# Performance work log

Hardware: AMD Instinct MI355X
Metric: run time of the kernel (lower is better)

The kernel has to match this reference:

```python
import jax, jax.numpy as jnp
import numpy as np

# dims: batch N, queries Q, frames F, patches-per-frame L, heads H, head_dim D
N, Q, F, L, H, D = 32, 64, 16, 196, 12, 64
E = H * D          # embed_dim = 768
K = F * L          # kv length = 3136


def setup_inputs() -> dict:
    key = jax.random.key(0)
    kq, kk, kv, km, kw1, kw2 = jax.random.split(key, 6)
    q = jax.random.normal(kq, (N, Q, E), dtype=jnp.float32)
    k = jax.random.normal(kk, (N, K, H, D), dtype=jnp.float32)
    v = jax.random.normal(kv, (N, K, H, D), dtype=jnp.float32)
    # frame-padding mask; guarantee >=1 valid patch per frame so the
    # per-frame softmax never sees an all -inf group (NaN otherwise)
    m = jax.random.bernoulli(km, 0.9, (N, K))
    m = m.reshape(N, F, L).at[:, :, 0].set(True).reshape(N, K)
    W_in = jax.random.normal(kw1, (E, E), dtype=jnp.float32) * 0.02   # in_proj (n_act=1)
    W_out = jax.random.normal(kw2, (E, E), dtype=jnp.float32) * 0.02  # out_proj
    return {"q": q, "k": k, "v": v, "m": m, "W_in": W_in, "W_out": W_out}


def reference(q, k, v, m, W_in, W_out):
    n, nq, e = q.shape
    h, d = H, e // H
    # in_proj (no bias) then split into heads; n_act == 1 so qs has one element
    qs = (q @ W_in.T).reshape(n, nq, h, d)
    # scaled QK affinity: [n, Q, K, h]
    aff = jnp.einsum('nqhc,nkhc->nqkh', qs * (d ** -0.5), k)
    # frame mask broadcast over queries and heads
    aff = jnp.where(m[:, None, :, None], aff, -jnp.inf)
    kn = aff.shape[2]
    # grouped softmax over patches within each frame (dim=-2 of the view)
    aff = jax.nn.softmax(aff.reshape(n, nq, F, kn // F, h), axis=-2)
    aff = aff.reshape(n, nq, kn, h)
    # mix with v and output projection
    mix = jnp.einsum('nqlh,nlhc->nqhc', aff, v)
    out = mix.reshape(n, nq, e) @ W_out.T
    # second return: stacked flattened qs, shape [n, n_act=1, Q, E]
    qs_out = qs.reshape(n, nq, e)[:, None]
    return out, qs_out
```

## Files before the change

### kernel.cpp

```cpp
#include <hip/hip_runtime.h>
#include <hip/hip_bf16.h>
#include <cfloat>

#define N_B 32
#define QN 64
#define FN 16
#define LP 196
#define HN 12
#define DH 64
#define EE 768
#define KLEN 3136
#define FPB 2
#define KROWS 208
#define VST 256

typedef short s16x4 __attribute__((ext_vector_type(4)));
typedef __bf16 bf16x8 __attribute__((ext_vector_type(8)));
typedef float f32x4 __attribute__((ext_vector_type(4)));
typedef unsigned u32x4 __attribute__((ext_vector_type(4)));

__device__ __forceinline__ bf16x8 cvt8(f32x4 a, f32x4 b) {
    bf16x8 r;
    r[0] = (__bf16)a[0]; r[1] = (__bf16)a[1]; r[2] = (__bf16)a[2]; r[3] = (__bf16)a[3];
    r[4] = (__bf16)b[0]; r[5] = (__bf16)b[1]; r[6] = (__bf16)b[2]; r[7] = (__bf16)b[3];
    return r;
}
__device__ __forceinline__ unsigned short bfb(float x) {
    return __builtin_bit_cast(unsigned short, (__bf16)x);
}
__device__ __forceinline__ unsigned pkbf(float lo, float hi) {
    return (unsigned)bfb(lo) | ((unsigned)bfb(hi) << 16);
}

__global__ __launch_bounds__(256) void gemm_mfma(const float* __restrict__ A,
                                                 const float* __restrict__ W,
                                                 float* __restrict__ C) {
    __shared__ unsigned short As[64 * 72];
    __shared__ unsigned short Ws[48 * 72];
    const int t = threadIdx.x;
    const int w = t >> 6, lane = t & 63, lr = lane & 15, lg = lane >> 4;
    const int m0 = blockIdx.x * 64;
    const int n0 = blockIdx.y * 48;

    f32x4 acc[3];
#pragma unroll
    for (int ct = 0; ct < 3; ++ct) acc[ct] = (f32x4){0.f, 0.f, 0.f, 0.f};

    for (int k0 = 0; k0 < EE; k0 += 32) {
        {
            int row = t >> 2, cb = t & 3;
            const float* src = A + (size_t)(m0 + row) * EE + k0 + cb * 8;
            f32x4 a = *(const f32x4*)src, b = *(const f32x4*)(src + 4);
            *(bf16x8*)&As[row * 72 + cb * 8] = cvt8(a, b);
        }
        if (t < 192) {
            int row = t >> 2, cb = t & 3;
            const float* src = W + (size_t)(n0 + row) * EE + k0 + cb * 8;
            f32x4 a = *(const f32x4*)src, b = *(const f32x4*)(src + 4);
            *(bf16x8*)&Ws[row * 72 + cb * 8] = cvt8(a, b);
        }
        __syncthreads();
        bf16x8 a = *(const bf16x8*)&As[(w * 16 + lr) * 72 + lg * 8];
#pragma unroll
        for (int ct = 0; ct < 3; ++ct) {
            bf16x8 b = *(const bf16x8*)&Ws[(ct * 16 + lr) * 72 + lg * 8];
            acc[ct] = __builtin_amdgcn_mfma_f32_16x16x32_bf16(a, b, acc[ct], 0, 0, 0);
        }
        __syncthreads();
    }
#pragma unroll
    for (int ct = 0; ct < 3; ++ct)
#pragma unroll
        for (int r = 0; r < 4; ++r)
            C[(size_t)(m0 + w * 16 + lg * 4 + r) * EE + n0 + ct * 16 + lr] = acc[ct][r];
}

__global__ __launch_bounds__(256) void zero_f32(float* __restrict__ p, int n4) {
    int i = blockIdx.x * 256 + threadIdx.x;
    if (i < n4) ((float4*)p)[i] = make_float4(0.f, 0.f, 0.f, 0.f);
}

__global__ __launch_bounds__(256, 2) void attn_mfma(const float* __restrict__ qs_g,
                                                    const float* __restrict__ k_g,
                                                    const float* __restrict__ v_g,
                                                    const int* __restrict__ m_g,
                                                    float* __restrict__ mix_g) {
    const int h = blockIdx.x, fg = blockIdx.y, n = blockIdx.z;

    __shared__ __attribute__((aligned(16))) unsigned short KV_s[64 * VST];
    __shared__ __attribute__((aligned(16))) float bias_s[224];

    const int t = threadIdx.x;
    const int w = t >> 6, lane = t & 63, lr = lane & 15, lg = lane >> 4;

    bf16x8 qb0, qb1;
    {
        const float* qp = qs_g + ((size_t)n * QN + w * 16 + lr) * EE + h * DH + lg * 8;
        f32x4 a = *(const f32x4*)qp, b = *(const f32x4*)(qp + 4);
        f32x4 c = *(const f32x4*)(qp + 32), d = *(const f32x4*)(qp + 36);
#pragma unroll
        for (int i = 0; i < 4; ++i) { a[i] *= 0.125f; b[i] *= 0.125f; c[i] *= 0.125f; d[i] *= 0.125f; }
        qb0 = cvt8(a, b);
        qb1 = cvt8(c, d);
    }

    float mix[4][4];
#pragma unroll
    for (int dt = 0; dt < 4; ++dt)
#pragma unroll
        for (int r = 0; r < 4; ++r) mix[dt][r] = 0.f;

    for (int ff = 0; ff < FPB; ++ff) {
        const size_t kbase = (size_t)n * KLEN + (size_t)(fg * FPB + ff) * LP;

        __syncthreads();

#pragma unroll
        for (int u = 0; u < 7; ++u) {
            int unit = t + 256 * u;
            if (unit < KROWS * 8) {
                int p = unit >> 3, blk = unit & 7;
                f32x4 a = {0.f, 0.f, 0.f, 0.f}, b = {0.f, 0.f, 0.f, 0.f};
                if (p < LP) {
                    const float* src = k_g + ((kbase + p) * HN + h) * DH + blk * 8;
                    a = *(const f32x4*)src;
                    b = *(const f32x4*)(src + 4);
                }
                *(bf16x8*)&KV_s[p * 64 + ((blk ^ (p & 7)) << 3)] = cvt8(a, b);
            }
        }
        if (t < 224) {
            float bv = -1e30f;
            if (t < LP && m_g[kbase + t] != 0) bv = 0.f;
            bias_s[t] = bv;
        }
        __syncthreads();

        f32x4 sc[13];
#pragma unroll
        for (int tl = 0; tl < 13; ++tl) {
            int row = tl * 16 + lr;
            bf16x8 a0 = *(const bf16x8*)&KV_s[row * 64 + ((lg ^ (lr & 7)) << 3)];
            bf16x8 a1 = *(const bf16x8*)&KV_s[row * 64 + (((4 + lg) ^ (lr & 7)) << 3)];
            f32x4 z = {0.f, 0.f, 0.f, 0.f};
            z = __builtin_amdgcn_mfma_f32_16x16x32_bf16(a0, qb0, z, 0, 0, 0);
            sc[tl] = __builtin_amdgcn_mfma_f32_16x16x32_bf16(a1, qb1, z, 0, 0, 0);
        }

        float mx = -FLT_MAX;
#pragma unroll
        for (int tl = 0; tl < 13; ++tl) {
            f32x4 bv = *(const f32x4*)&bias_s[tl * 16 + lg * 4];
#pragma unroll
            for (int r = 0; r < 4; ++r) {
                float sv = sc[tl][r] + bv[r];
                sc[tl][r] = sv;
                mx = fmaxf(mx, sv);
            }
        }
        mx = fmaxf(mx, __shfl_xor(mx, 16));
        mx = fmaxf(mx, __shfl_xor(mx, 32));
        float sum = 0.f;
        unsigned pk[14][2];
#pragma unroll
        for (int tl = 0; tl < 13; ++tl) {
            float e0 = __expf(sc[tl][0] - mx);
            float e1 = __expf(sc[tl][1] - mx);
            float e2 = __expf(sc[tl][2] - mx);
            float e3 = __expf(sc[tl][3] - mx);
            sum += (e0 + e1) + (e2 + e3);
            pk[tl][0] = pkbf(e0, e1);
            pk[tl][1] = pkbf(e2, e3);
        }
        pk[13][0] = 0u; pk[13][1] = 0u;
        sum += __shfl_xor(sum, 16);
        sum += __shfl_xor(sum, 32);
        float inv = 1.0f / sum;
        float li[4];
#pragma unroll
        for (int r = 0; r < 4; ++r) li[r] = __shfl(inv, lg * 4 + r);

        __syncthreads();

#pragma unroll
        for (int u = 0; u < 7; ++u) {
            int unit = t + 256 * u;
            int pp = unit >> 4, d4 = unit & 15;
            int p0 = pp * 2;
            f32x4 va = {0.f, 0.f, 0.f, 0.f}, vb = {0.f, 0.f, 0.f, 0.f};
            if (p0 < LP) {
                const float* vg = v_g + ((kbase + p0) * HN + h) * DH + d4 * 4;
                va = *(const f32x4*)vg;
                if (p0 + 1 < LP) vb = *(const f32x4*)(vg + (size_t)HN * DH);
            }
            int blk = p0 >> 3, sub = p0 & 7;
#pragma unroll
            for (int i = 0; i < 4; ++i) {
                int row = d4 * 4 + i;
                int g = (row + 2 * (row >> 2)) & 7;
                *(unsigned*)&KV_s[row * VST + (((blk ^ g) << 3) | sub)] = pkbf(va[i], vb[i]);
            }
        }
        __syncthreads();

        f32x4 pv[4];
#pragma unroll
        for (int dt = 0; dt < 4; ++dt) pv[dt] = (f32x4){0.f, 0.f, 0.f, 0.f};
        const bool lgb0 = (lg & 1) != 0, lgb1 = (lg >> 1) != 0;
#pragma unroll
        for (int ks = 0; ks < 7; ++ks) {
            unsigned a0 = pk[2 * ks][0],     a1 = pk[2 * ks][1];
            unsigned b0 = pk[2 * ks + 1][0], b1 = pk[2 * ks + 1][1];
            unsigned xA0 = __shfl_xor(a0, 16), xA1 = __shfl_xor(a1, 16);
            unsigned yA0 = __shfl_xor(a0, 32), yA1 = __shfl_xor(a1, 32);
            unsigned zA0 = __shfl_xor(a0, 48), zA1 = __shfl_xor(a1, 48);
            unsigned xB0 = __shfl_xor(b0, 16), xB1 = __shfl_xor(b1, 16);
            unsigned yB0 = __shfl_xor(b0, 32), yB1 = __shfl_xor(b1, 32);
            unsigned zB0 = __shfl_xor(b0, 48), zB1 = __shfl_xor(b1, 48);
            unsigned s0 = lgb1 ? (lgb0 ? xB0 : yB0) : (lgb0 ? zA0 : a0);
            unsigned s1 = lgb1 ? (lgb0 ? xB1 : yB1) : (lgb0 ? zA1 : a1);
            unsigned s2 = lgb1 ? (lgb0 ? b0 : zB0) : (lgb0 ? yA0 : xA0);
            unsigned s3 = lgb1 ? (lgb0 ? b1 : zB1) : (lgb0 ? yA1 : xA1);
            bf16x8 pa = __builtin_bit_cast(bf16x8, (u32x4){s0, s1, s2, s3});
#pragma unroll
            for (int dt = 0; dt < 4; ++dt) {
                int row = dt * 16 + lr;
                int g = (row + 2 * (row >> 2)) & 7;
                bf16x8 b = *(const bf16x8*)&KV_s[row * VST + ((((ks * 4 + lg) ^ g)) << 3)];
                pv[dt] = __builtin_amdgcn_mfma_f32_16x16x32_bf16(pa, b, pv[dt], 0, 0, 0);
            }
        }
#pragma unroll
        for (int dt = 0; dt < 4; ++dt)
#pragma unroll
            for (int r = 0; r < 4; ++r) mix[dt][r] += pv[dt][r] * li[r];
    }

#pragma unroll
    for (int dt = 0; dt < 4; ++dt)
#pragma unroll
        for (int r = 0; r < 4; ++r)
            atomicAdd(mix_g + ((size_t)n * QN + w * 16 + lg * 4 + r) * EE + h * DH + dt * 16 + lr,
                      mix[dt][r]);
}

extern "C" void kernel_launch(void* const* d_in, const int* in_sizes, int n_in,
                              void* d_out, int out_size, void* d_ws, size_t ws_size,
                              hipStream_t stream) {
    const float* q  = (const float*)d_in[0];
    const float* k  = (const float*)d_in[1];
    const float* v  = (const float*)d_in[2];
    const int*   m  = (const int*)d_in[3];
    const float* Wi = (const float*)d_in[4];
    const float* Wo = (const float*)d_in[5];

    float* out = (float*)d_out;
    float* qs  = out + (size_t)N_B * QN * EE;
    float* mix = (float*)d_ws;

    const int mix_n4 = (N_B * QN * EE) / 4;
    dim3 ggrid((N_B * QN) / 64, EE / 48);
    gemm_mfma<<<ggrid, 256, 0, stream>>>(q, Wi, qs);
    zero_f32<<<(mix_n4 + 255) / 256, 256, 0, stream>>>(mix, mix_n4);
    attn_mfma<<<dim3(HN, FN / FPB, N_B), 256, 0, stream>>>(qs, k, v, m, mix);
    gemm_mfma<<<ggrid, 256, 0, stream>>>(mix, Wo, out);
}
```

Baseline: 240.6 us.

## Split V staging into halves, prefetch V during softmax, use 16x16x16 MFMA

The V tile is now loaded in two halves. The first half is prefetched into registers right after the QK MFMAs so the global load overlaps the softmax. The PV product switches from the 16x16x32 MFMA, which needed cross-lane shuffles to rearrange P, to 16x16x16 bf16 MFMAs that consume the packed P registers directly. The second half of V is loaded while the first-half PV runs, and s_setprio hints wrap the MFMA phases. In exchange it adds an extra barrier, holds more registers for the prefetched V, and issues twice as many smaller MFMAs.

```diff
diff --git a/kernel.cpp b/kernel.cpp
--- a/kernel.cpp
+++ b/kernel.cpp
@@ -15,9 +15,10 @@
 #define VST 256
 
 typedef short s16x4 __attribute__((ext_vector_type(4)));
+typedef __bf16 bf16x4 __attribute__((ext_vector_type(4)));
 typedef __bf16 bf16x8 __attribute__((ext_vector_type(8)));
 typedef float f32x4 __attribute__((ext_vector_type(4)));
-typedef unsigned u32x4 __attribute__((ext_vector_type(4)));
+typedef unsigned u32x2 __attribute__((ext_vector_type(2)));
 
 __device__ __forceinline__ bf16x8 cvt8(f32x4 a, f32x4 b) {
     bf16x8 r;
@@ -30,6 +31,20 @@
 }
 __device__ __forceinline__ unsigned pkbf(float lo, float hi) {
     return (unsigned)bfb(lo) | ((unsigned)bfb(hi) << 16);
+}
+
+__device__ __forceinline__ f32x4 mfma16(s16x4 a, s16x4 b, f32x4 c) {
+#if __has_builtin(__builtin_amdgcn_mfma_f32_16x16x16_bf16)
+    return __builtin_amdgcn_mfma_f32_16x16x16_bf16(__builtin_bit_cast(bf16x4, a),
+                                                   __builtin_bit_cast(bf16x4, b), c, 0, 0, 0);
+#elif __has_builtin(__builtin_amdgcn_mfma_f32_16x16x16bf16_1k)
+    return __builtin_amdgcn_mfma_f32_16x16x16bf16_1k(a, b, c, 0, 0, 0);
+#else
+    f32x4 d;
+    asm volatile("v_mfma_f32_16x16x16_bf16 %0, %1, %2, %3"
+                 : "=v"(d) : "v"(a), "v"(b), "v"(c));
+    return d;
+#endif
 }
 
 __global__ __launch_bounds__(256) void gemm_mfma(const float* __restrict__ A,
@@ -137,6 +152,7 @@
         __syncthreads();
 
         f32x4 sc[13];
+        __builtin_amdgcn_s_setprio(1);
 #pragma unroll
         for (int tl = 0; tl < 13; ++tl) {
             int row = tl * 16 + lr;
@@ -146,6 +162,22 @@
             z = __builtin_amdgcn_mfma_f32_16x16x32_bf16(a0, qb0, z, 0, 0, 0);
             sc[tl] = __builtin_amdgcn_mfma_f32_16x16x32_bf16(a1, qb1, z, 0, 0, 0);
         }
+        __builtin_amdgcn_s_setprio(0);
+
+        f32x4 va[4], vb[4];
+#pragma unroll
+        for (int u = 0; u < 4; ++u) {
+            int unit = t + 256 * u;
+            int pp = unit >> 3, d4 = unit & 7;
+            int p0 = pp * 2;
+            va[u] = (f32x4){0.f, 0.f, 0.f, 0.f};
+            vb[u] = (f32x4){0.f, 0.f, 0.f, 0.f};
+            if (p0 < LP) {
+                const float* vg = v_g + ((kbase + p0) * HN + h) * DH + d4 * 4;
+                va[u] = *(const f32x4*)vg;
+                if (p0 + 1 < LP) vb[u] = *(const f32x4*)(vg + (size_t)HN * DH);
+            }
+        }
 
         float mx = -FLT_MAX;
 #pragma unroll
@@ -161,7 +193,7 @@
         mx = fmaxf(mx, __shfl_xor(mx, 16));
         mx = fmaxf(mx, __shfl_xor(mx, 32));
         float sum = 0.f;
-        unsigned pk[14][2];
+        unsigned pk[13][2];
 #pragma unroll
         for (int tl = 0; tl < 13; ++tl) {
             float e0 = __expf(sc[tl][0] - mx);
@@ -172,7 +204,6 @@
             pk[tl][0] = pkbf(e0, e1);
             pk[tl][1] = pkbf(e2, e3);
         }
-        pk[13][0] = 0u; pk[13][1] = 0u;
         sum += __shfl_xor(sum, 16);
         sum += __shfl_xor(sum, 32);
         float inv = 1.0f / sum;
@@ -183,22 +214,31 @@
         __syncthreads();
 
 #pragma unroll
-        for (int u = 0; u < 7; ++u) {
-            int unit = t + 256 * u;
-            int pp = unit >> 4, d4 = unit & 15;
+        for (int u = 0; u < 4; ++u) {
+            int unit = t + 256 * u;
+            int pp = unit >> 3, d4 = unit & 7;
             int p0 = pp * 2;
-            f32x4 va = {0.f, 0.f, 0.f, 0.f}, vb = {0.f, 0.f, 0.f, 0.f};
+            if (p0 < KROWS) {
+                int blk = p0 >> 3, sub = p0 & 7;
+#pragma unroll
+                for (int i = 0; i < 4; ++i) {
+                    int row = d4 * 4 + i;
+                    int g = (row + 2 * (row >> 2)) & 7;
+                    *(unsigned*)&KV_s[row * VST + (((blk ^ g) << 3) | sub)] = pkbf(va[u][i], vb[u][i]);
+                }
+            }
+        }
+#pragma unroll
+        for (int u = 0; u < 4; ++u) {
+            int unit = t + 256 * u;
+            int pp = unit >> 3, d4 = unit & 7;
+            int p0 = pp * 2;
+            va[u] = (f32x4){0.f, 0.f, 0.f, 0.f};
+            vb[u] = (f32x4){0.f, 0.f, 0.f, 0.f};
             if (p0 < LP) {
-                const float* vg = v_g + ((kbase + p0) * HN + h) * DH + d4 * 4;
-                va = *(const f32x4*)vg;
-                if (p0 + 1 < LP) vb = *(const f32x4*)(vg + (size_t)HN * DH);
-            }
-            int blk = p0 >> 3, sub = p0 & 7;
-#pragma unroll
-            for (int i = 0; i < 4; ++i) {
-                int row = d4 * 4 + i;
-                int g = (row + 2 * (row >> 2)) & 7;
-                *(unsigned*)&KV_s[row * VST + (((blk ^ g) << 3) | sub)] = pkbf(va[i], vb[i]);
+                const float* vg = v_g + ((kbase + p0) * HN + h) * DH + (8 + d4) * 4;
+                va[u] = *(const f32x4*)vg;
+                if (p0 + 1 < LP) vb[u] = *(const f32x4*)(vg + (size_t)HN * DH);
             }
         }
         __syncthreads();
@@ -206,30 +246,53 @@
         f32x4 pv[4];
 #pragma unroll
         for (int dt = 0; dt < 4; ++dt) pv[dt] = (f32x4){0.f, 0.f, 0.f, 0.f};
-        const bool lgb0 = (lg & 1) != 0, lgb1 = (lg >> 1) != 0;
-#pragma unroll
-        for (int ks = 0; ks < 7; ++ks) {
-            unsigned a0 = pk[2 * ks][0],     a1 = pk[2 * ks][1];
-            unsigned b0 = pk[2 * ks + 1][0], b1 = pk[2 * ks + 1][1];
-            unsigned xA0 = __shfl_xor(a0, 16), xA1 = __shfl_xor(a1, 16);
-            unsigned yA0 = __shfl_xor(a0, 32), yA1 = __shfl_xor(a1, 32);
-            unsigned zA0 = __shfl_xor(a0, 48), zA1 = __shfl_xor(a1, 48);
-            unsigned xB0 = __shfl_xor(b0, 16), xB1 = __shfl_xor(b1, 16);
-            unsigned yB0 = __shfl_xor(b0, 32), yB1 = __shfl_xor(b1, 32);
-            unsigned zB0 = __shfl_xor(b0, 48), zB1 = __shfl_xor(b1, 48);
-            unsigned s0 = lgb1 ? (lgb0 ? xB0 : yB0) : (lgb0 ? zA0 : a0);
-            unsigned s1 = lgb1 ? (lgb0 ? xB1 : yB1) : (lgb0 ? zA1 : a1);
-            unsigned s2 = lgb1 ? (lgb0 ? b0 : zB0) : (lgb0 ? yA0 : xA0);
-            unsigned s3 = lgb1 ? (lgb0 ? b1 : zB1) : (lgb0 ? yA1 : xA1);
-            bf16x8 pa = __builtin_bit_cast(bf16x8, (u32x4){s0, s1, s2, s3});
-#pragma unroll
-            for (int dt = 0; dt < 4; ++dt) {
-                int row = dt * 16 + lr;
-                int g = (row + 2 * (row >> 2)) & 7;
-                bf16x8 b = *(const bf16x8*)&KV_s[row * VST + ((((ks * 4 + lg) ^ g)) << 3)];
-                pv[dt] = __builtin_amdgcn_mfma_f32_16x16x32_bf16(pa, b, pv[dt], 0, 0, 0);
-            }
-        }
+        __builtin_amdgcn_s_setprio(1);
+#pragma unroll
+        for (int dt = 0; dt < 2; ++dt) {
+            int row = dt * 16 + lr;
+            int g = (row + 2 * (row >> 2)) & 7;
+#pragma unroll
+            for (int kt = 0; kt < 13; ++kt) {
+                int c0 = kt * 16 + lg * 4;
+                s16x4 b = *(const s16x4*)&KV_s[row * VST + ((((c0 >> 3) ^ g) << 3) | (c0 & 7))];
+                s16x4 a = __builtin_bit_cast(s16x4, (u32x2){pk[kt][0], pk[kt][1]});
+                pv[dt] = mfma16(a, b, pv[dt]);
+            }
+        }
+        __builtin_amdgcn_s_setprio(0);
+
+#pragma unroll
+        for (int u = 0; u < 4; ++u) {
+            int unit = t + 256 * u;
+            int pp = unit >> 3, d4 = unit & 7;
+            int p0 = pp * 2;
+            if (p0 < KROWS) {
+                int blk = p0 >> 3, sub = p0 & 7;
+#pragma unroll
+                for (int i = 0; i < 4; ++i) {
+                    int row = 32 + d4 * 4 + i;
+                    int g = (row + 2 * (row >> 2)) & 7;
+                    *(unsigned*)&KV_s[row * VST + (((blk ^ g) << 3) | sub)] = pkbf(va[u][i], vb[u][i]);
+                }
+            }
+        }
+        __syncthreads();
+
+        __builtin_amdgcn_s_setprio(1);
+#pragma unroll
+        for (int dt = 2; dt < 4; ++dt) {
+            int row = dt * 16 + lr;
+            int g = (row + 2 * (row >> 2)) & 7;
+#pragma unroll
+            for (int kt = 0; kt < 13; ++kt) {
+                int c0 = kt * 16 + lg * 4;
+                s16x4 b = *(const s16x4*)&KV_s[row * VST + ((((c0 >> 3) ^ g) << 3) | (c0 & 7))];
+                s16x4 a = __builtin_bit_cast(s16x4, (u32x2){pk[kt][0], pk[kt][1]});
+                pv[dt] = mfma16(a, b, pv[dt]);
+            }
+        }
+        __builtin_amdgcn_s_setprio(0);
+
 #pragma unroll
         for (int dt = 0; dt < 4; ++dt)
 #pragma unroll
```

Result: faster. 218.0 us (-9.4%).
